# Performance work log

Measured on AMD Instinct MI355X. Metric: run time of the kernel, lower is better.

## Reference

```python
import jax, jax.numpy as jnp
import numpy as np

HIDDEN = 2048
HEAD_DIM = 256
N_HEADS = 8
N_KV_HEADS = 2
N_GROUPS = N_HEADS // N_KV_HEADS
EPS = 1e-6
WAVELENGTH = 10000.0
ROPE_SCALE = 1.0
NEG_INF = -1e9


def setup_inputs() -> dict:
    key = jax.random.key(0)
    ks = jax.random.split(key, 8)
    B, S = 2, 2048
    hidden_states = jax.random.normal(ks[0], (B, S, HIDDEN), dtype=jnp.float32)
    # additive causal mask: 0 on/below diagonal, -1e9 above
    causal = jnp.tril(jnp.ones((S, S), dtype=bool))
    attention_mask = jnp.where(causal, 0.0, NEG_INF).astype(jnp.float32)[None, None]
    attention_mask = jnp.broadcast_to(attention_mask, (B, 1, S, S))
    sd = 1.0 / np.sqrt(HIDDEN)
    wq = jax.random.normal(ks[1], (HIDDEN, N_HEADS * HEAD_DIM), dtype=jnp.float32) * sd
    wk = jax.random.normal(ks[2], (HIDDEN, N_KV_HEADS * HEAD_DIM), dtype=jnp.float32) * sd
    wv = jax.random.normal(ks[3], (HIDDEN, N_KV_HEADS * HEAD_DIM), dtype=jnp.float32) * sd
    wo = jax.random.normal(ks[4], (N_HEADS * HEAD_DIM, HIDDEN), dtype=jnp.float32) * (1.0 / np.sqrt(N_HEADS * HEAD_DIM))
    q_scale = 1.0 + 0.02 * jax.random.normal(ks[5], (HEAD_DIM,), dtype=jnp.float32)
    k_scale = 1.0 + 0.02 * jax.random.normal(ks[6], (HEAD_DIM,), dtype=jnp.float32)
    return {"hidden_states": hidden_states, "attention_mask": attention_mask,
            "wq": wq, "wk": wk, "wv": wv, "wo": wo,
            "q_scale": q_scale, "k_scale": k_scale}


def _rms_norm(x, scale=None):
    # Gemma3nRMSNorm: compute in float32, optional scale, cast back
    x32 = x.astype(jnp.float32)
    out = x32 * jax.lax.rsqrt(jnp.mean(x32 * x32, axis=-1, keepdims=True) + EPS)
    if scale is not None:
        out = out * scale.astype(jnp.float32)
    return out.astype(x.dtype)


def _rope(x, start_index=0):
    # x: [B, S, H, D]; keras-hub RotaryEmbedding (half-split rotate)
    S, D = x.shape[1], x.shape[-1]
    inv_freq = 1.0 / (WAVELENGTH ** (jnp.arange(0, D, 2, dtype=jnp.float32) / D))
    pos = (jnp.arange(S, dtype=jnp.float32) + start_index) / ROPE_SCALE
    freq = jnp.einsum("s,f->sf", pos, inv_freq)           # [S, D/2]
    emb = jnp.concatenate([freq, freq], axis=-1)          # [S, D]
    cos = jnp.cos(emb)[None, :, None, :].astype(x.dtype)
    sin = jnp.sin(emb)[None, :, None, :].astype(x.dtype)
    x1, x2 = jnp.split(x, 2, axis=-1)
    rot = jnp.concatenate([-x2, x1], axis=-1)
    return x * cos + rot * sin


def reference(hidden_states, attention_mask, wq, wk, wv, wo, q_scale, k_scale):
    B, S, _ = hidden_states.shape
    q = (hidden_states @ wq).reshape(B, S, N_HEADS, HEAD_DIM)
    k = (hidden_states @ wk).reshape(B, S, N_KV_HEADS, HEAD_DIM)
    v = (hidden_states @ wv).reshape(B, S, N_KV_HEADS, HEAD_DIM)
    q = _rope(_rms_norm(q, q_scale))
    k = _rope(_rms_norm(k, k_scale))
    v = _rms_norm(v)  # with_scale=False
    # GQA: repeat KV heads, then BHSD layout
    k = jnp.repeat(k, N_GROUPS, axis=2)
    v = jnp.repeat(v, N_GROUPS, axis=2)
    q = q.transpose(0, 2, 1, 3)
    k = k.transpose(0, 2, 1, 3)
    v = v.transpose(0, 2, 1, 3)
    scores = jnp.einsum("bhqd,bhkd->bhqk", q, k) / np.sqrt(HEAD_DIM)
    scores = scores + attention_mask.astype(scores.dtype)
    probs = jax.nn.softmax(scores.astype(jnp.float32), axis=-1).astype(hidden_states.dtype)
    out = jnp.einsum("bhqk,bhkd->bhqd", probs, v)
    out = out.transpose(0, 2, 1, 3).reshape(B, S, N_HEADS * HEAD_DIM)
    return out @ wo
```

## Files before the change

### kernel.cpp

```cpp
#include <hip/hip_runtime.h>
#include <cstdint>
#include <cstddef>

#define SEQ   2048
#define BATCH 2
#define NH    8
#define NKV   2
#define DH    256
#define HID   2048
#define MR    (BATCH*SEQ)

typedef _Float16 h8 __attribute__((ext_vector_type(8)));
typedef _Float16 h4 __attribute__((ext_vector_type(4)));
typedef float   f32x4 __attribute__((ext_vector_type(4)));
typedef int     i32x4 __attribute__((ext_vector_type(4)));

__device__ __forceinline__ f32x4 mfma16(h8 a, h8 b, f32x4 c) {
  return __builtin_amdgcn_mfma_f32_16x16x32_f16(a, b, c, 0, 0, 0);
}
__device__ __forceinline__ void gload16(const void* g, void* l) {
  __builtin_amdgcn_global_load_lds((__attribute__((address_space(1))) void*)g,
                                   (__attribute__((address_space(3))) void*)l,
                                   16, 0, 0);
}
__device__ __forceinline__ int pkf16(float a, float b) {
  auto t = __builtin_amdgcn_cvt_pkrtz(a, b);
  return __builtin_bit_cast(int, t);
}

__global__ __launch_bounds__(256) void cvt_f16(const float* __restrict__ in,
                                               _Float16* __restrict__ out, int n4) {
  const int i = blockIdx.x * 256 + threadIdx.x;
  if (i >= n4) return;
  const float4 v = ((const float4*)in)[i];
  h4 o = { (_Float16)v.x, (_Float16)v.y, (_Float16)v.z, (_Float16)v.w };
  ((h4*)out)[i] = o;
}

__global__ __launch_bounds__(256) void wtrans(const float* __restrict__ in,
                                              _Float16* __restrict__ out,
                                              int N, int K) {
  __shared__ float L[32][33];
  const int n0 = blockIdx.x * 32, k0 = blockIdx.y * 32;
  const int t = threadIdx.x;
  const int r = t >> 3, c4 = (t & 7) * 4;
  const float4 v = *(const float4*)&in[(size_t)(k0 + r) * N + n0 + c4];
  L[r][c4] = v.x; L[r][c4 + 1] = v.y; L[r][c4 + 2] = v.z; L[r][c4 + 3] = v.w;
  __syncthreads();
  h4 o = { (_Float16)L[c4][r], (_Float16)L[c4 + 1][r],
           (_Float16)L[c4 + 2][r], (_Float16)L[c4 + 3][r] };
  *(h4*)&out[(size_t)(n0 + r) * K + k0 + c4] = o;
}

__global__ __launch_bounds__(256) void gemm_f16(const _Float16* __restrict__ A,
                                                const _Float16* __restrict__ Bt,
                                                float* __restrict__ C,
                                                const int N, const int K) {
  __shared__ __align__(16) unsigned char sm[32768];
  const int t = threadIdx.x, w = t >> 6, lane = t & 63;
  const int l15 = lane & 15, l4 = lane >> 4;
  const int wr = w >> 1, wc = w & 1;
  const int m0 = blockIdx.y * 128, n0 = blockIdx.x * 128;
  const int swz = (l15 & 7) << 4;
  const size_t rb = (size_t)K * 2;

  int rS[4], cS[4];
#pragma unroll
  for (int i = 0; i < 4; ++i) {
    const int o = i * 4096 + w * 1024 + lane * 16;
    rS[i] = o >> 7;
    cS[i] = (o & 127) ^ ((rS[i] & 7) << 4);
  }
  const char* Ab = (const char*)A + (size_t)m0 * rb;
  const char* Bb = (const char*)Bt + (size_t)n0 * rb;

  f32x4 acc[4][4] = {};

  for (int k0 = 0; k0 < K; k0 += 64) {
    __syncthreads();
#pragma unroll
    for (int i = 0; i < 4; ++i) {
      gload16(Ab + (size_t)rS[i] * rb + k0 * 2 + cS[i], sm + i * 4096 + w * 1024);
      gload16(Bb + (size_t)rS[i] * rb + k0 * 2 + cS[i], sm + 16384 + i * 4096 + w * 1024);
    }
    __syncthreads();
#pragma unroll
    for (int kk = 0; kk < 2; ++kk) {
      const int ko = (kk * 64 + l4 * 16) ^ swz;
      h8 av[4], bv[4];
#pragma unroll
      for (int f = 0; f < 4; ++f) {
        av[f] = *(const h8*)(sm + (wr * 64 + f * 16 + l15) * 128 + ko);
        bv[f] = *(const h8*)(sm + 16384 + (wc * 64 + f * 16 + l15) * 128 + ko);
      }
#pragma unroll
      for (int i = 0; i < 4; ++i)
#pragma unroll
        for (int j = 0; j < 4; ++j)
          acc[i][j] = mfma16(av[i], bv[j], acc[i][j]);
    }
  }
#pragma unroll
  for (int i = 0; i < 4; ++i)
#pragma unroll
    for (int r = 0; r < 4; ++r) {
      const int row = m0 + wr * 64 + i * 16 + l4 * 4 + r;
      float* Cp = C + (size_t)row * N + n0 + wc * 64 + l15;
#pragma unroll
      for (int j = 0; j < 4; ++j) Cp[j * 16] = acc[i][j][r];
    }
}

__global__ __launch_bounds__(256) void norm_rope_q(const float* __restrict__ QKVp,
                                                   _Float16* __restrict__ Qh,
                                                   const float* __restrict__ q_scale) {
  const int idx = blockIdx.x;
  const int t = threadIdx.x;
  const int h = idx & 7;
  const int bs = idx >> 3;
  const int s = bs & (SEQ - 1);
  const int b = bs >> 11;
  const float x = QKVp[(size_t)bs * 3072 + h * 256 + t];
  float ss = x * x;
#pragma unroll
  for (int off = 32; off; off >>= 1) ss += __shfl_xor(ss, off);
  __shared__ float red[4];
  if ((t & 63) == 0) red[t >> 6] = ss;
  __syncthreads();
  const float tot = red[0] + red[1] + red[2] + red[3];
  const float inv = rsqrtf(tot * (1.0f / 256.0f) + 1e-6f);
  const float xn = x * inv * q_scale[t];
  __shared__ float rowbuf[256];
  rowbuf[t] = xn;
  __syncthreads();
  const int f = t & 127;
  const float invf = expf(-0.07195578415606391f * (float)f);
  float sn, cs;
  sincosf((float)s * invf, &sn, &cs);
  const float other = rowbuf[t ^ 128];
  const float o = (t < 128) ? (xn * cs - other * sn) : (xn * cs + other * sn);
  Qh[((size_t)(b * NH + h) * SEQ + s) * DH + t] = (_Float16)(o * 0.0625f);
}

__global__ __launch_bounds__(256) void norm_kv(const float* __restrict__ QKVp,
                                               _Float16* __restrict__ Kh,
                                               _Float16* __restrict__ Vh,
                                               const float* __restrict__ k_scale) {
  const int idx = blockIdx.x;
  const int t = threadIdx.x;
  const bool isK = idx < 8192;
  const int i = isK ? idx : idx - 8192;
  const int kv = i & 1;
  const int bs = i >> 1;
  const int s = bs & (SEQ - 1);
  const int b = bs >> 11;
  const int col = (isK ? 2048 + kv * DH : 2560 + kv * DH) + t;
  const float x = QKVp[(size_t)bs * 3072 + col];
  float ss = x * x;
#pragma unroll
  for (int off = 32; off; off >>= 1) ss += __shfl_xor(ss, off);
  __shared__ float red[4];
  if ((t & 63) == 0) red[t >> 6] = ss;
  __syncthreads();
  const float tot = red[0] + red[1] + red[2] + red[3];
  const float inv = rsqrtf(tot * (1.0f / 256.0f) + 1e-6f);
  float xn = x * inv;
  const size_t o = ((size_t)(b * NKV + kv) * SEQ + s) * DH + t;
  if (isK) {
    xn *= k_scale[t];
    __shared__ float rowbuf[256];
    rowbuf[t] = xn;
    __syncthreads();
    const int f = t & 127;
    const float invf = expf(-0.07195578415606391f * (float)f);
    float sn, cs;
    sincosf((float)s * invf, &sn, &cs);
    const float other = rowbuf[t ^ 128];
    const float ov = (t < 128) ? (xn * cs - other * sn) : (xn * cs + other * sn);
    Kh[o] = (_Float16)ov;
  } else {
    Vh[o] = (_Float16)xn;
  }
}

__global__ __launch_bounds__(256) void transpose_v(const _Float16* __restrict__ Vh,
                                                   _Float16* __restrict__ Vt) {
  __shared__ _Float16 L[32][36];
  const int s0 = blockIdx.x * 32, d0 = blockIdx.y * 32;
  const size_t base = (size_t)blockIdx.z * SEQ * DH;
  const int t = threadIdx.x;
  const int r = t >> 3, c4 = (t & 7) * 4;
  const h4 v = *(const h4*)&Vh[base + (size_t)(s0 + r) * DH + d0 + c4];
  L[r][c4] = v.x; L[r][c4 + 1] = v.y; L[r][c4 + 2] = v.z; L[r][c4 + 3] = v.w;
  __syncthreads();
  h4 o = { L[c4][r], L[c4 + 1][r], L[c4 + 2][r], L[c4 + 3][r] };
  *(h4*)&Vt[base + (size_t)(d0 + r) * SEQ + s0 + c4] = o;
}

__global__ __launch_bounds__(256, 2) void attn_f16(const _Float16* __restrict__ Qh,
                                                   const _Float16* __restrict__ Kh,
                                                   const _Float16* __restrict__ Vt,
                                                   _Float16* __restrict__ Ah) {
  __shared__ __align__(16) unsigned char sm[65536];
  const int pid = blockIdx.x;
  const int h = blockIdx.y, b = blockIdx.z;
  const int kh = h >> 2;
  const int qt = b ? (31 - pid) : pid;
  const int q0 = qt * 64;
  const int t = threadIdx.x, w = t >> 6, lane = t & 63;
  const int l15 = lane & 15, l4 = lane >> 4;
  const int swz = (l15 & 7) << 4;

  const char* Qg = (const char*)(Qh + (size_t)(b * NH + h) * SEQ * DH);
  const char* Kg = (const char*)(Kh + (size_t)(b * NKV + kh) * SEQ * DH);
  const char* Vg = (const char*)(Vt + (size_t)(b * NKV + kh) * DH * SEQ);

#pragma unroll
  for (int i = 0; i < 8; ++i) {
    const int o = i * 4096 + w * 1024 + lane * 16;
    const int row = o >> 9;
    const int off = (o & 511) ^ ((row & 7) << 4);
    gload16(Qg + (size_t)(q0 + row) * 512 + off, sm + i * 4096 + w * 1024);
  }
  __syncthreads();
  h8 qf[8];
  {
    const int qrow = w * 16 + l15;
#pragma unroll
    for (int dc = 0; dc < 8; ++dc)
      qf[dc] = *(const h8*)(sm + qrow * 512 + ((dc * 64 + l4 * 16) ^ swz));
  }
  f32x4 o_acc[16] = {};
  float mrun = -3e38f, lrun = 0.f;

  for (int kt = 0; kt <= qt; ++kt) {
    __syncthreads();
#pragma unroll
    for (int i = 0; i < 8; ++i) {
      const int o = i * 4096 + w * 1024 + lane * 16;
      const int row = o >> 9;
      const int off = (o & 511) ^ ((row & 7) << 4);
      gload16(Kg + (size_t)(kt * 64 + row) * 512 + off, sm + i * 4096 + w * 1024);
      const int d = o >> 7;
      const int voff = (o & 127) ^ ((d & 7) << 4);
      gload16(Vg + (size_t)d * (SEQ * 2) + kt * 128 + voff,
              sm + 32768 + i * 4096 + w * 1024);
    }
    __syncthreads();

    f32x4 sc[4];
    __builtin_amdgcn_s_setprio(1);
#pragma unroll
    for (int fk = 0; fk < 4; ++fk) {
      f32x4 z = {};
      sc[fk] = z;
      const int krow = fk * 16 + l15;
#pragma unroll
      for (int dc = 0; dc < 8; ++dc) {
        const h8 kf = *(const h8*)(sm + krow * 512 + ((dc * 64 + l4 * 16) ^ swz));
        sc[fk] = mfma16(kf, qf[dc], sc[fk]);
      }
    }
    __builtin_amdgcn_s_setprio(0);

    float e[4][4];
    if (kt == qt) {
#pragma unroll
      for (int fk = 0; fk < 4; ++fk)
#pragma unroll
        for (int r = 0; r < 4; ++r)
          e[fk][r] = (fk * 16 + l4 * 4 + r <= w * 16 + l15) ? sc[fk][r] : -3e38f;
    } else {
#pragma unroll
      for (int fk = 0; fk < 4; ++fk)
#pragma unroll
        for (int r = 0; r < 4; ++r) e[fk][r] = sc[fk][r];
    }
    float pm = -3e38f;
#pragma unroll
    for (int fk = 0; fk < 4; ++fk)
#pragma unroll
      for (int r = 0; r < 4; ++r) pm = fmaxf(pm, e[fk][r]);
    pm = fmaxf(pm, __shfl_xor(pm, 16));
    pm = fmaxf(pm, __shfl_xor(pm, 32));
    const float mnew = fmaxf(mrun, pm);
    const float alpha = __expf(mrun - mnew);
    mrun = mnew;
    float ls = 0.f;
#pragma unroll
    for (int fk = 0; fk < 4; ++fk)
#pragma unroll
      for (int r = 0; r < 4; ++r) {
        e[fk][r] = __expf(e[fk][r] - mnew);
        ls += e[fk][r];
      }
    ls += __shfl_xor(ls, 16);
    ls += __shfl_xor(ls, 32);
    lrun = lrun * alpha + ls;

    float al[4];
#pragma unroll
    for (int r = 0; r < 4; ++r) al[r] = __shfl(alpha, l4 * 4 + r);
#pragma unroll
    for (int fd = 0; fd < 16; ++fd)
#pragma unroll
      for (int r = 0; r < 4; ++r) o_acc[fd][r] *= al[r];

    h8 pa[2];
    const int src0 = l15 + ((l4 & 1) << 5);
    const int src1 = src0 + 16;
    const bool lowk = (l4 < 2);
#pragma unroll
    for (int kk = 0; kk < 2; ++kk) {
      const int d0 = pkf16(e[2 * kk][0], e[2 * kk][1]);
      const int d1 = pkf16(e[2 * kk][2], e[2 * kk][3]);
      const int d2 = pkf16(e[2 * kk + 1][0], e[2 * kk + 1][1]);
      const int d3 = pkf16(e[2 * kk + 1][2], e[2 * kk + 1][3]);
      const int s00 = __shfl(d0, src0);
      const int s10 = __shfl(d1, src0);
      const int s20 = __shfl(d2, src0);
      const int s30 = __shfl(d3, src0);
      const int s01 = __shfl(d0, src1);
      const int s11 = __shfl(d1, src1);
      const int s21 = __shfl(d2, src1);
      const int s31 = __shfl(d3, src1);
      const int n0 = lowk ? s00 : s20;
      const int n1 = lowk ? s10 : s30;
      const int n2 = lowk ? s01 : s21;
      const int n3 = lowk ? s11 : s31;
      i32x4 pw = { n0, n1, n2, n3 };
      pa[kk] = __builtin_bit_cast(h8, pw);
    }

    __builtin_amdgcn_s_setprio(1);
#pragma unroll
    for (int kk = 0; kk < 2; ++kk) {
      const int ko = (kk * 64 + l4 * 16) ^ swz;
#pragma unroll
      for (int fd = 0; fd < 16; ++fd) {
        const h8 vf = *(const h8*)(sm + 32768 + (fd * 16 + l15) * 128 + ko);
        o_acc[fd] = mfma16(pa[kk], vf, o_acc[fd]);
      }
    }
    __builtin_amdgcn_s_setprio(0);
  }

  const float inv = 1.0f / lrun;
#pragma unroll
  for (int r = 0; r < 4; ++r) {
    const float linv = __shfl(inv, l4 * 4 + r);
    const int srow = q0 + w * 16 + l4 * 4 + r;
    _Float16* Op = Ah + (size_t)(b * SEQ + srow) * (NH * DH) + h * DH + l15;
#pragma unroll
    for (int fd = 0; fd < 16; ++fd)
      Op[fd * 16] = (_Float16)(o_acc[fd][r] * linv);
  }
}

extern "C" void kernel_launch(void* const* d_in, const int* in_sizes, int n_in,
                              void* d_out, int out_size, void* d_ws, size_t ws_size,
                              hipStream_t stream) {
  (void)in_sizes; (void)n_in; (void)out_size; (void)ws_size;
  const float* hidden  = (const float*)d_in[0];
  const float* wq      = (const float*)d_in[2];
  const float* wk      = (const float*)d_in[3];
  const float* wv      = (const float*)d_in[4];
  const float* wo      = (const float*)d_in[5];
  const float* q_scale = (const float*)d_in[6];
  const float* k_scale = (const float*)d_in[7];
  float* out = (float*)d_out;

  uint8_t* ws = (uint8_t*)d_ws;
  _Float16* hid_h = (_Float16*)ws;  ws += (size_t)MR * HID * 2;
  _Float16* Wt    = (_Float16*)ws;  ws += (size_t)3072 * HID * 2;
  float*    QKVp  = (float*)ws;     ws += (size_t)MR * 3072 * 4;
  _Float16* Qh    = (_Float16*)ws;  ws += (size_t)MR * HID * 2;
  _Float16* Kh    = (_Float16*)ws;  ws += (size_t)MR * 512 * 2;
  _Float16* Vh    = (_Float16*)ws;  ws += (size_t)MR * 512 * 2;
  _Float16* Vt    = (_Float16*)ws;  ws += (size_t)MR * 512 * 2;
  _Float16* Ah    = (_Float16*)QKVp;

  const dim3 blk(256);
  cvt_f16<<<dim3(8192), blk, 0, stream>>>(hidden, hid_h, MR * HID / 4);
  wtrans<<<dim3(64, 64), blk, 0, stream>>>(wq, Wt, 2048, 2048);
  wtrans<<<dim3(16, 64), blk, 0, stream>>>(wk, Wt + (size_t)2048 * 2048, 512, 2048);
  wtrans<<<dim3(16, 64), blk, 0, stream>>>(wv, Wt + (size_t)2560 * 2048, 512, 2048);
  gemm_f16<<<dim3(24, 32), blk, 0, stream>>>(hid_h, Wt, QKVp, 3072, 2048);
  wtrans<<<dim3(64, 64), blk, 0, stream>>>(wo, Wt, 2048, 2048);
  norm_rope_q<<<dim3(32768), blk, 0, stream>>>(QKVp, Qh, q_scale);
  norm_kv<<<dim3(16384), blk, 0, stream>>>(QKVp, Kh, Vh, k_scale);
  transpose_v<<<dim3(64, 8, 4), blk, 0, stream>>>(Vh, Vt);
  attn_f16<<<dim3(32, 8, 2), blk, 0, stream>>>(Qh, Kh, Vt, Ah);
  gemm_f16<<<dim3(16, 32), blk, 0, stream>>>(Ah, Wt, out, 2048, 2048);
}
```

Measured before the change: 395.0 us.

## Restructure attention: 128-row Q tiles, 32-row KV tiles, double-buffered LDS staging

The attention kernel now gives each block 128 query rows (two 16-row groups per wave) and streams K/V in 32-row tiles through two LDS buffers, prefetching the next tile while computing the current one. Q fragments are loaded straight from global memory instead of through LDS. The change aims to hide global-load latency and reuse each K/V fragment across two query groups. In exchange, per-wave register use roughly doubles (occupancy drops to one block per CU), the grid halves to 256 blocks, and the batch-reversed load balancing of causal tiles is removed.

```diff
diff --git a/kernel.cpp b/kernel.cpp
--- a/kernel.cpp
+++ b/kernel.cpp
@@ -197,163 +197,170 @@
   *(h4*)&Vt[base + (size_t)(d0 + r) * SEQ + s0 + c4] = o;
 }
 
-__global__ __launch_bounds__(256, 2) void attn_f16(const _Float16* __restrict__ Qh,
+__global__ __launch_bounds__(256, 1) void attn_f16(const _Float16* __restrict__ Qh,
                                                    const _Float16* __restrict__ Kh,
                                                    const _Float16* __restrict__ Vt,
                                                    _Float16* __restrict__ Ah) {
   __shared__ __align__(16) unsigned char sm[65536];
-  const int pid = blockIdx.x;
+  const int qt = blockIdx.x;
   const int h = blockIdx.y, b = blockIdx.z;
   const int kh = h >> 2;
-  const int qt = b ? (31 - pid) : pid;
-  const int q0 = qt * 64;
+  const int q0 = qt * 128;
+  const int nt = 4 * (qt + 1);
   const int t = threadIdx.x, w = t >> 6, lane = t & 63;
   const int l15 = lane & 15, l4 = lane >> 4;
-  const int swz = (l15 & 7) << 4;
+  const int swzk = (l15 & 7) << 4;
+  const int swzv = (l15 & 3) << 4;
 
   const char* Qg = (const char*)(Qh + (size_t)(b * NH + h) * SEQ * DH);
   const char* Kg = (const char*)(Kh + (size_t)(b * NKV + kh) * SEQ * DH);
   const char* Vg = (const char*)(Vt + (size_t)(b * NKV + kh) * DH * SEQ);
 
-#pragma unroll
-  for (int i = 0; i < 8; ++i) {
-    const int o = i * 4096 + w * 1024 + lane * 16;
-    const int row = o >> 9;
-    const int off = (o & 511) ^ ((row & 7) << 4);
-    gload16(Qg + (size_t)(q0 + row) * 512 + off, sm + i * 4096 + w * 1024);
-  }
-  __syncthreads();
-  h8 qf[8];
-  {
-    const int qrow = w * 16 + l15;
-#pragma unroll
-    for (int dc = 0; dc < 8; ++dc)
-      qf[dc] = *(const h8*)(sm + qrow * 512 + ((dc * 64 + l4 * 16) ^ swz));
-  }
-  f32x4 o_acc[16] = {};
-  float mrun = -3e38f, lrun = 0.f;
-
-  for (int kt = 0; kt <= qt; ++kt) {
-    __syncthreads();
-#pragma unroll
-    for (int i = 0; i < 8; ++i) {
+  auto stage_tile = [&](int kt, int p) {
+    unsigned char* Kb = sm + p * 32768;
+    unsigned char* Vb = Kb + 16384;
+#pragma unroll
+    for (int i = 0; i < 4; ++i) {
       const int o = i * 4096 + w * 1024 + lane * 16;
       const int row = o >> 9;
-      const int off = (o & 511) ^ ((row & 7) << 4);
-      gload16(Kg + (size_t)(kt * 64 + row) * 512 + off, sm + i * 4096 + w * 1024);
-      const int d = o >> 7;
-      const int voff = (o & 127) ^ ((d & 7) << 4);
-      gload16(Vg + (size_t)d * (SEQ * 2) + kt * 128 + voff,
-              sm + 32768 + i * 4096 + w * 1024);
+      const int koff = (o & 511) ^ ((row & 7) << 4);
+      gload16(Kg + (size_t)(kt * 32 + row) * 512 + koff, Kb + i * 4096 + w * 1024);
+      const int d = o >> 6;
+      const int voff = (o & 63) ^ ((d & 3) << 4);
+      gload16(Vg + (size_t)d * (SEQ * 2) + kt * 64 + voff, Vb + i * 4096 + w * 1024);
+    }
+  };
+
+  stage_tile(0, 0);
+
+  h8 qf[2][8];
+#pragma unroll
+  for (int g = 0; g < 2; ++g) {
+    const int qrow = q0 + w * 32 + g * 16 + l15;
+#pragma unroll
+    for (int dc = 0; dc < 8; ++dc)
+      qf[g][dc] = *(const h8*)(Qg + (size_t)qrow * 512 + dc * 64 + l4 * 16);
+  }
+
+  f32x4 o_acc[2][16] = {};
+  float mrun[2] = { -3e38f, -3e38f };
+  float lrun[2] = { 0.f, 0.f };
+  __syncthreads();
+
+  for (int kt = 0; kt < nt; ++kt) {
+    const int p = kt & 1;
+    if (kt + 1 < nt) stage_tile(kt + 1, p ^ 1);
+
+    if (kt * 32 <= q0 + w * 32 + 31) {
+      const unsigned char* Kb = sm + p * 32768;
+      const unsigned char* Vb = Kb + 16384;
+
+      f32x4 sc[2][2];
+#pragma unroll
+      for (int fk = 0; fk < 2; ++fk) {
+        f32x4 a0 = {}, a1 = {};
+        const int krow = fk * 16 + l15;
+#pragma unroll
+        for (int dc = 0; dc < 8; ++dc) {
+          const h8 kf = *(const h8*)(Kb + krow * 512 + ((dc * 64 + l4 * 16) ^ swzk));
+          a0 = mfma16(kf, qf[0][dc], a0);
+          a1 = mfma16(kf, qf[1][dc], a1);
+        }
+        sc[0][fk] = a0; sc[1][fk] = a1;
+      }
+
+      h8 pa[2];
+#pragma unroll
+      for (int g = 0; g < 2; ++g) {
+        const int qlo = q0 + w * 32 + g * 16;
+        const int qrow = qlo + l15;
+        float e[2][4];
+        if (kt * 32 + 31 > qlo) {
+#pragma unroll
+          for (int fk = 0; fk < 2; ++fk)
+#pragma unroll
+            for (int r = 0; r < 4; ++r)
+              e[fk][r] = (kt * 32 + fk * 16 + l4 * 4 + r <= qrow) ? sc[g][fk][r]
+                                                                  : -3e38f;
+        } else {
+#pragma unroll
+          for (int fk = 0; fk < 2; ++fk)
+#pragma unroll
+            for (int r = 0; r < 4; ++r) e[fk][r] = sc[g][fk][r];
+        }
+        float pm = -3e38f;
+#pragma unroll
+        for (int fk = 0; fk < 2; ++fk)
+#pragma unroll
+          for (int r = 0; r < 4; ++r) pm = fmaxf(pm, e[fk][r]);
+        pm = fmaxf(pm, __shfl_xor(pm, 16));
+        pm = fmaxf(pm, __shfl_xor(pm, 32));
+        const float mnew = fmaxf(mrun[g], pm);
+        const float alpha = __expf(mrun[g] - mnew);
+        mrun[g] = mnew;
+        float ls = 0.f;
+#pragma unroll
+        for (int fk = 0; fk < 2; ++fk)
+#pragma unroll
+          for (int r = 0; r < 4; ++r) {
+            e[fk][r] = __expf(e[fk][r] - mnew);
+            ls += e[fk][r];
+          }
+        ls += __shfl_xor(ls, 16);
+        ls += __shfl_xor(ls, 32);
+        lrun[g] = lrun[g] * alpha + ls;
+
+        float al[4];
+#pragma unroll
+        for (int r = 0; r < 4; ++r) al[r] = __shfl(alpha, l4 * 4 + r);
+#pragma unroll
+        for (int fd = 0; fd < 16; ++fd)
+#pragma unroll
+          for (int r = 0; r < 4; ++r) o_acc[g][fd][r] *= al[r];
+
+        const int d0 = pkf16(e[0][0], e[0][1]);
+        const int d1 = pkf16(e[0][2], e[0][3]);
+        const int d2 = pkf16(e[1][0], e[1][1]);
+        const int d3 = pkf16(e[1][2], e[1][3]);
+        const int src0 = l15 + ((l4 & 1) << 5);
+        const int src1 = src0 + 16;
+        const bool lowk = (l4 < 2);
+        const int s00 = __shfl(d0, src0);
+        const int s10 = __shfl(d1, src0);
+        const int s20 = __shfl(d2, src0);
+        const int s30 = __shfl(d3, src0);
+        const int s01 = __shfl(d0, src1);
+        const int s11 = __shfl(d1, src1);
+        const int s21 = __shfl(d2, src1);
+        const int s31 = __shfl(d3, src1);
+        i32x4 pw = { lowk ? s00 : s20, lowk ? s10 : s30,
+                     lowk ? s01 : s21, lowk ? s11 : s31 };
+        pa[g] = __builtin_bit_cast(h8, pw);
+      }
+
+      const int ko = (l4 * 16) ^ swzv;
+#pragma unroll
+      for (int fd = 0; fd < 16; ++fd) {
+        const h8 vf = *(const h8*)(Vb + (fd * 16 + l15) * 64 + ko);
+        o_acc[0][fd] = mfma16(pa[0], vf, o_acc[0][fd]);
+        o_acc[1][fd] = mfma16(pa[1], vf, o_acc[1][fd]);
+      }
     }
     __syncthreads();
-
-    f32x4 sc[4];
-    __builtin_amdgcn_s_setprio(1);
-#pragma unroll
-    for (int fk = 0; fk < 4; ++fk) {
-      f32x4 z = {};
-      sc[fk] = z;
-      const int krow = fk * 16 + l15;
-#pragma unroll
-      for (int dc = 0; dc < 8; ++dc) {
-        const h8 kf = *(const h8*)(sm + krow * 512 + ((dc * 64 + l4 * 16) ^ swz));
-        sc[fk] = mfma16(kf, qf[dc], sc[fk]);
-      }
-    }
-    __builtin_amdgcn_s_setprio(0);
-
-    float e[4][4];
-    if (kt == qt) {
-#pragma unroll
-      for (int fk = 0; fk < 4; ++fk)
-#pragma unroll
-        for (int r = 0; r < 4; ++r)
-          e[fk][r] = (fk * 16 + l4 * 4 + r <= w * 16 + l15) ? sc[fk][r] : -3e38f;
-    } else {
-#pragma unroll
-      for (int fk = 0; fk < 4; ++fk)
-#pragma unroll
-        for (int r = 0; r < 4; ++r) e[fk][r] = sc[fk][r];
-    }
-    float pm = -3e38f;
-#pragma unroll
-    for (int fk = 0; fk < 4; ++fk)
-#pragma unroll
-      for (int r = 0; r < 4; ++r) pm = fmaxf(pm, e[fk][r]);
-    pm = fmaxf(pm, __shfl_xor(pm, 16));
-    pm = fmaxf(pm, __shfl_xor(pm, 32));
-    const float mnew = fmaxf(mrun, pm);
-    const float alpha = __expf(mrun - mnew);
-    mrun = mnew;
-    float ls = 0.f;
-#pragma unroll
-    for (int fk = 0; fk < 4; ++fk)
-#pragma unroll
-      for (int r = 0; r < 4; ++r) {
-        e[fk][r] = __expf(e[fk][r] - mnew);
-        ls += e[fk][r];
-      }
-    ls += __shfl_xor(ls, 16);
-    ls += __shfl_xor(ls, 32);
-    lrun = lrun * alpha + ls;
-
-    float al[4];
-#pragma unroll
-    for (int r = 0; r < 4; ++r) al[r] = __shfl(alpha, l4 * 4 + r);
-#pragma unroll
-    for (int fd = 0; fd < 16; ++fd)
-#pragma unroll
-      for (int r = 0; r < 4; ++r) o_acc[fd][r] *= al[r];
-
-    h8 pa[2];
-    const int src0 = l15 + ((l4 & 1) << 5);
-    const int src1 = src0 + 16;
-    const bool lowk = (l4 < 2);
-#pragma unroll
-    for (int kk = 0; kk < 2; ++kk) {
-      const int d0 = pkf16(e[2 * kk][0], e[2 * kk][1]);
-      const int d1 = pkf16(e[2 * kk][2], e[2 * kk][3]);
-      const int d2 = pkf16(e[2 * kk + 1][0], e[2 * kk + 1][1]);
-      const int d3 = pkf16(e[2 * kk + 1][2], e[2 * kk + 1][3]);
-      const int s00 = __shfl(d0, src0);
-      const int s10 = __shfl(d1, src0);
-      const int s20 = __shfl(d2, src0);
-      const int s30 = __shfl(d3, src0);
-      const int s01 = __shfl(d0, src1);
-      const int s11 = __shfl(d1, src1);
-      const int s21 = __shfl(d2, src1);
-      const int s31 = __shfl(d3, src1);
-      const int n0 = lowk ? s00 : s20;
-      const int n1 = lowk ? s10 : s30;
-      const int n2 = lowk ? s01 : s21;
-      const int n3 = lowk ? s11 : s31;
-      i32x4 pw = { n0, n1, n2, n3 };
-      pa[kk] = __builtin_bit_cast(h8, pw);
-    }
-
-    __builtin_amdgcn_s_setprio(1);
-#pragma unroll
-    for (int kk = 0; kk < 2; ++kk) {
-      const int ko = (kk * 64 + l4 * 16) ^ swz;
-#pragma unroll
-      for (int fd = 0; fd < 16; ++fd) {
-        const h8 vf = *(const h8*)(sm + 32768 + (fd * 16 + l15) * 128 + ko);
-        o_acc[fd] = mfma16(pa[kk], vf, o_acc[fd]);
-      }
-    }
-    __builtin_amdgcn_s_setprio(0);
-  }
-
-  const float inv = 1.0f / lrun;
-#pragma unroll
-  for (int r = 0; r < 4; ++r) {
-    const float linv = __shfl(inv, l4 * 4 + r);
-    const int srow = q0 + w * 16 + l4 * 4 + r;
-    _Float16* Op = Ah + (size_t)(b * SEQ + srow) * (NH * DH) + h * DH + l15;
-#pragma unroll
-    for (int fd = 0; fd < 16; ++fd)
-      Op[fd * 16] = (_Float16)(o_acc[fd][r] * linv);
+  }
+
+#pragma unroll
+  for (int g = 0; g < 2; ++g) {
+    const float inv = 1.0f / lrun[g];
+#pragma unroll
+    for (int r = 0; r < 4; ++r) {
+      const float linv = __shfl(inv, l4 * 4 + r);
+      const int srow = q0 + w * 32 + g * 16 + l4 * 4 + r;
+      _Float16* Op = Ah + (size_t)(b * SEQ + srow) * (NH * DH) + h * DH + l15;
+#pragma unroll
+      for (int fd = 0; fd < 16; ++fd)
+        Op[fd * 16] = (_Float16)(o_acc[g][fd][r] * linv);
+    }
   }
 }
 
@@ -390,6 +397,6 @@
   norm_rope_q<<<dim3(32768), blk, 0, stream>>>(QKVp, Qh, q_scale);
   norm_kv<<<dim3(16384), blk, 0, stream>>>(QKVp, Kh, Vh, k_scale);
   transpose_v<<<dim3(64, 8, 4), blk, 0, stream>>>(Vh, Vt);
-  attn_f16<<<dim3(32, 8, 2), blk, 0, stream>>>(Qh, Kh, Vt, Ah);
+  attn_f16<<<dim3(16, 8, 2), blk, 0, stream>>>(Qh, Kh, Vt, Ah);
   gemm_f16<<<dim3(16, 32), blk, 0, stream>>>(Ah, Wt, out, 2048, 2048);
 }
```

Measured after the change: 473.0 us. 1.2x slower.
